# Performance work log

Hardware: AMD Instinct MI355X
Metric: run time of the kernel (lower is better)

The kernel has to match this reference:

```python
import math
import jax, jax.numpy as jnp
import numpy as np

D_MODEL = 1024
N_HEADS = 16
HEAD_DIM = D_MODEL // N_HEADS
D_FF = 4096
N_LAYERS = 4
VOCAB = 2048
NUM_GROUPS = 15
CACHE_LEN = 17  # positions 0..16
EPS = 1e-6


def rmsnorm(x, w):
    return x * w * jax.lax.rsqrt(jnp.mean(x * x, axis=-1, keepdims=True) + EPS)


def rope(x, pos):
    # x: [S, H, hd], pos: [S] int
    hd = x.shape[-1]
    inv = 1.0 / (10000.0 ** (jnp.arange(0, hd, 2, dtype=jnp.float32) / hd))
    ang = pos[:, None].astype(jnp.float32) * inv  # [S, hd/2]
    cos = jnp.cos(ang)[:, None, :]
    sin = jnp.sin(ang)[:, None, :]
    x1, x2 = x[..., ::2], x[..., 1::2]
    return jnp.stack([x1 * cos - x2 * sin, x1 * sin + x2 * cos], axis=-1).reshape(x.shape)


def transformer_step(x, positions, kc, vc, wq, wk, wv, wo, w1, w2, w3, ln1, ln2, lnf):
    # x: [S, d]; positions: [S] contiguous; kc/vc: [L, H, T, hd] KV caches
    S = x.shape[0]
    cache_pos = jnp.arange(CACHE_LEN)
    mask = cache_pos[None, None, :] <= positions[None, :, None]  # causal vs cache [1,S,T]
    start = positions[0]
    for l in range(N_LAYERS):
        h = rmsnorm(x, ln1[l])
        q = rope((h @ wq[l].T).reshape(S, N_HEADS, HEAD_DIM), positions)
        k = rope((h @ wk[l].T).reshape(S, N_HEADS, HEAD_DIM), positions)
        v = (h @ wv[l].T).reshape(S, N_HEADS, HEAD_DIM)
        kc = jax.lax.dynamic_update_slice(kc, k.transpose(1, 0, 2)[None], (l, 0, start, 0))
        vc = jax.lax.dynamic_update_slice(vc, v.transpose(1, 0, 2)[None], (l, 0, start, 0))
        scores = jnp.einsum('shd,htd->hst', q, kc[l]) / math.sqrt(HEAD_DIM)
        p = jax.nn.softmax(jnp.where(mask, scores, -1e30), axis=-1)
        attn = jnp.einsum('hst,htd->shd', p, vc[l]).reshape(S, D_MODEL)
        x = x + attn @ wo[l].T
        h = rmsnorm(x, ln2[l])
        x = x + (jax.nn.silu(h @ w1[l].T) * (h @ w3[l].T)) @ w2[l].T
    return rmsnorm(x, lnf), kc, vc


def forward(talker_hidden, code_0_embed, wq, wk, wv, wo, w1, w2, w3, ln1, ln2, lnf, heads, embeds):
    kc = jnp.zeros((N_LAYERS, N_HEADS, CACHE_LEN, HEAD_DIM), jnp.float32)
    vc = kc
    # prefill: [talker_hidden; code_0_embed] at positions 0,1
    x0 = jnp.concatenate([talker_hidden[0], code_0_embed[0]], axis=0)  # [2, d]
    h, kc, vc = transformer_step(x0, jnp.arange(2), kc, vc, wq, wk, wv, wo, w1, w2, w3, ln1, ln2, lnf)
    hidden = h[-1:]  # last-token hidden [1, d]

    def step(carry, xs):
        hidden, kc, vc = carry
        head, etab, pos = xs  # head/etab: [V, d]
        logits = hidden @ head.T          # [1, V]
        code = jnp.argmax(logits, axis=-1)  # [1]
        emb = etab[code]                   # [1, d]
        nh, kc, vc = transformer_step(emb, pos[None], kc, vc, wq, wk, wv, wo, w1, w2, w3, ln1, ln2, lnf)
        return (nh, kc, vc), (logits[0], emb[0])

    (_, _, _), (all_logits, embs) = jax.lax.scan(
        step, (hidden, kc, vc), (heads, embeds, jnp.arange(2, 2 + NUM_GROUPS)))
    embed_sum = code_0_embed.reshape(-1) + embs.sum(0)
    return all_logits, embed_sum  # [15, V], [d]


def setup_inputs() -> dict:
    key = jax.random.key(0)
    ks = jax.random.split(key, 16)
    s = 0.02
    f32 = jnp.float32
    return {
        'talker_hidden': jax.random.normal(ks[0], (1, 1, D_MODEL), f32),
        'code_0_embed': jax.random.normal(ks[1], (1, 1, D_MODEL), f32),
        'wq': jax.random.normal(ks[2], (N_LAYERS, D_MODEL, D_MODEL), f32) * s,
        'wk': jax.random.normal(ks[3], (N_LAYERS, D_MODEL, D_MODEL), f32) * s,
        'wv': jax.random.normal(ks[4], (N_LAYERS, D_MODEL, D_MODEL), f32) * s,
        'wo': jax.random.normal(ks[5], (N_LAYERS, D_MODEL, D_MODEL), f32) * s,
        'w1': jax.random.normal(ks[6], (N_LAYERS, D_FF, D_MODEL), f32) * s,
        'w2': jax.random.normal(ks[7], (N_LAYERS, D_MODEL, D_FF), f32) * s,
        'w3': jax.random.normal(ks[8], (N_LAYERS, D_FF, D_MODEL), f32) * s,
        'ln1': jnp.ones((N_LAYERS, D_MODEL), f32),
        'ln2': jnp.ones((N_LAYERS, D_MODEL), f32),
        'lnf': jnp.ones((D_MODEL,), f32),
        'heads': jax.random.normal(ks[9], (NUM_GROUPS, VOCAB, D_MODEL), f32) * s,
        'embeds': jax.random.normal(ks[10], (NUM_GROUPS, VOCAB, D_MODEL), f32) * s,
    }


def reference(talker_hidden, code_0_embed, wq, wk, wv, wo, w1, w2, w3, ln1, ln2, lnf, heads, embeds):
    return forward(talker_hidden, code_0_embed, wq, wk, wv, wo, w1, w2, w3, ln1, ln2, lnf, heads, embeds)
```

## Files before the change

### kernel.cpp

```cpp
#include <hip/hip_runtime.h>
#include <hip/hip_bf16.h>
#include <math.h>

#define D_MODEL 1024
#define N_HEADS 16
#define HEAD_DIM 64
#define D_FF 4096
#define N_LAYERS 4
#define VOCAB 2048
#define NUM_GROUPS 15
#define CACHE_LEN 17
#define EPS 1e-6f

typedef unsigned short ushort8v __attribute__((ext_vector_type(8)));

__device__ __forceinline__ float bf2f(unsigned short u) {
  union { unsigned int i; float f; } c;
  c.i = ((unsigned int)u) << 16;
  return c.f;
}

__device__ __forceinline__ unsigned short f2bf(float f) {
  union { float f; unsigned int i; } c;
  c.f = f;
  unsigned int r = (c.i + 0x7fffu + ((c.i >> 16) & 1u)) >> 16;
  return (unsigned short)r;
}

__device__ __forceinline__ float wred(float v) {
#pragma unroll
  for (int o = 32; o > 0; o >>= 1) v += __shfl_xor(v, o, 64);
  return v;
}

template <int NT>
__device__ __forceinline__ void block_rms_scale(const float* __restrict__ x, int S,
                                                float* s_scale, float* s_tmp) {
  for (int s = 0; s < S; ++s) {
    float p = 0.f;
    for (int j = threadIdx.x; j < D_MODEL; j += NT) {
      float v = x[s * D_MODEL + j];
      p += v * v;
    }
    p = wred(p);
    if ((threadIdx.x & 63) == 0) s_tmp[threadIdx.x >> 6] = p;
    __syncthreads();
    if (threadIdx.x == 0) {
      float t = 0.f;
#pragma unroll
      for (int w = 0; w < NT / 64; ++w) t += s_tmp[w];
      s_scale[s] = rsqrtf(t / (float)D_MODEL + EPS);
    }
    __syncthreads();
  }
}

template <int NIT>
__device__ __forceinline__ void load_act_scaled(const float* __restrict__ x,
                                                const float* __restrict__ ln,
                                                float scale, float* a) {
  int lane = threadIdx.x & 63;
  const float4* xv = (const float4*)x;
  const float4* lv = (const float4*)ln;
#pragma unroll
  for (int it = 0; it < NIT; ++it) {
    float4 v0 = xv[it * 128 + lane * 2];
    float4 v1 = xv[it * 128 + lane * 2 + 1];
    float4 l0 = lv[it * 128 + lane * 2];
    float4 l1 = lv[it * 128 + lane * 2 + 1];
    a[it * 8 + 0] = v0.x * l0.x * scale;
    a[it * 8 + 1] = v0.y * l0.y * scale;
    a[it * 8 + 2] = v0.z * l0.z * scale;
    a[it * 8 + 3] = v0.w * l0.w * scale;
    a[it * 8 + 4] = v1.x * l1.x * scale;
    a[it * 8 + 5] = v1.y * l1.y * scale;
    a[it * 8 + 6] = v1.z * l1.z * scale;
    a[it * 8 + 7] = v1.w * l1.w * scale;
  }
}

template <typename WT, int NIT>
__device__ __forceinline__ float dot_cached(const WT* __restrict__ wrow, const float* a) {
  int lane = threadIdx.x & 63;
  float acc = 0.f;
  if constexpr (sizeof(WT) == 2) {
    const ushort8v* w8 = (const ushort8v*)wrow;
#pragma unroll
    for (int it = 0; it < NIT; ++it) {
      ushort8v w = w8[it * 64 + lane];
#pragma unroll
      for (int c = 0; c < 8; ++c) acc = fmaf(bf2f(w[c]), a[it * 8 + c], acc);
    }
  } else {
    const float4* w4 = (const float4*)wrow;
#pragma unroll
    for (int it = 0; it < NIT; ++it) {
      float4 b0 = w4[it * 128 + lane * 2];
      float4 b1 = w4[it * 128 + lane * 2 + 1];
      acc = fmaf(b0.x, a[it * 8 + 0], acc);
      acc = fmaf(b0.y, a[it * 8 + 1], acc);
      acc = fmaf(b0.z, a[it * 8 + 2], acc);
      acc = fmaf(b0.w, a[it * 8 + 3], acc);
      acc = fmaf(b1.x, a[it * 8 + 4], acc);
      acc = fmaf(b1.y, a[it * 8 + 5], acc);
      acc = fmaf(b1.z, a[it * 8 + 6], acc);
      acc = fmaf(b1.w, a[it * 8 + 7], acc);
    }
  }
  return wred(acc);
}

template <typename WT, int NIT>
__device__ __forceinline__ float dot_stream(const WT* __restrict__ wrow,
                                            const float* __restrict__ act) {
  int lane = threadIdx.x & 63;
  const float4* av = (const float4*)act;
  float acc = 0.f;
  if constexpr (sizeof(WT) == 2) {
    const ushort8v* w8 = (const ushort8v*)wrow;
#pragma unroll
    for (int it = 0; it < NIT; ++it) {
      ushort8v w = w8[it * 64 + lane];
      float4 v0 = av[it * 128 + lane * 2];
      float4 v1 = av[it * 128 + lane * 2 + 1];
      acc = fmaf(bf2f(w[0]), v0.x, acc);
      acc = fmaf(bf2f(w[1]), v0.y, acc);
      acc = fmaf(bf2f(w[2]), v0.z, acc);
      acc = fmaf(bf2f(w[3]), v0.w, acc);
      acc = fmaf(bf2f(w[4]), v1.x, acc);
      acc = fmaf(bf2f(w[5]), v1.y, acc);
      acc = fmaf(bf2f(w[6]), v1.z, acc);
      acc = fmaf(bf2f(w[7]), v1.w, acc);
    }
  } else {
    const float4* w4 = (const float4*)wrow;
#pragma unroll
    for (int it = 0; it < NIT; ++it) {
      float4 b0 = w4[it * 128 + lane * 2];
      float4 b1 = w4[it * 128 + lane * 2 + 1];
      float4 v0 = av[it * 128 + lane * 2];
      float4 v1 = av[it * 128 + lane * 2 + 1];
      acc = fmaf(b0.x, v0.x, acc);
      acc = fmaf(b0.y, v0.y, acc);
      acc = fmaf(b0.z, v0.z, acc);
      acc = fmaf(b0.w, v0.w, acc);
      acc = fmaf(b1.x, v1.x, acc);
      acc = fmaf(b1.y, v1.y, acc);
      acc = fmaf(b1.z, v1.z, acc);
      acc = fmaf(b1.w, v1.w, acc);
    }
  }
  return wred(acc);
}


__global__ void k_convert(const float* __restrict__ src, unsigned short* __restrict__ dst,
                          size_t n8) {
  size_t stride = (size_t)gridDim.x * blockDim.x;
  const float4* s4 = (const float4*)src;
  ushort8v* d8 = (ushort8v*)dst;
  for (size_t i = (size_t)blockIdx.x * blockDim.x + threadIdx.x; i < n8; i += stride) {
    float4 a = s4[2 * i];
    float4 b = s4[2 * i + 1];
    ushort8v o;
    o[0] = f2bf(a.x); o[1] = f2bf(a.y); o[2] = f2bf(a.z); o[3] = f2bf(a.w);
    o[4] = f2bf(b.x); o[5] = f2bf(b.y); o[6] = f2bf(b.z); o[7] = f2bf(b.w);
    d8[i] = o;
  }
}

__global__ void k_setup(const float* __restrict__ th, const float* __restrict__ c0,
                        float* __restrict__ x, float* __restrict__ esum) {
  int j = blockIdx.x * 256 + threadIdx.x;
  if (j < D_MODEL) {
    x[j] = th[j];
    x[D_MODEL + j] = c0[j];
    esum[j] = c0[j];
  }
}

template <typename WT>
__global__ __launch_bounds__(256) void k_qkv(
    const float* __restrict__ x, const float* __restrict__ ln,
    const WT* __restrict__ wq, const WT* __restrict__ wk, const WT* __restrict__ wv,
    float* __restrict__ qout, float* __restrict__ kcl, float* __restrict__ vcl,
    int S, int start) {
  __shared__ float s_scale[2];
  __shared__ float s_tmp[4];
  block_rms_scale<256>(x, S, s_scale, s_tmp);
  int lane = threadIdx.x & 63;
  int wid = blockIdx.x * 4 + (threadIdx.x >> 6);
  int m = wid >> 9;
  int p = wid & 511;
  const WT* W = (m == 0) ? wq : (m == 1) ? wk : wv;
  const WT* w0 = W + (size_t)(2 * p) * D_MODEL;
  const WT* w1 = w0 + D_MODEL;
  int h = (2 * p) >> 6;
  int dd = (2 * p) & 63;
  for (int s = 0; s < S; ++s) {
    float a[16];
    load_act_scaled<2>(x + s * D_MODEL, ln, s_scale[s], a);
    float d0 = dot_cached<WT, 2>(w0, a);
    float d1 = dot_cached<WT, 2>(w1, a);
    int pos = start + s;
    if (lane == 0) {
      if (m == 2) {
        vcl[(h * CACHE_LEN + pos) * HEAD_DIM + dd] = d0;
        vcl[(h * CACHE_LEN + pos) * HEAD_DIM + dd + 1] = d1;
      } else {
        int i = dd >> 1;
        float inv = powf(10000.f, -(float)(2 * i) / 64.f);
        float ang = (float)pos * inv;
        float c = cosf(ang), sn = sinf(ang);
        float o0 = d0 * c - d1 * sn;
        float o1 = d0 * sn + d1 * c;
        if (m == 0) {
          qout[s * D_MODEL + 2 * p] = o0;
          qout[s * D_MODEL + 2 * p + 1] = o1;
        } else {
          kcl[(h * CACHE_LEN + pos) * HEAD_DIM + dd] = o0;
          kcl[(h * CACHE_LEN + pos) * HEAD_DIM + dd + 1] = o1;
        }
      }
    }
  }
}

__global__ __launch_bounds__(64) void k_attn(const float* __restrict__ q,
                                             const float* __restrict__ kcl,
                                             const float* __restrict__ vcl,
                                             float* __restrict__ attnb, int S,
                                             int start) {
  int h = blockIdx.x;
  int lane = threadIdx.x;
  __shared__ float sp[CACHE_LEN];
  for (int s = 0; s < S; ++s) {
    int pos = start + s;
    float qd = q[s * D_MODEL + h * HEAD_DIM + lane];
    for (int t = 0; t <= pos; ++t) {
      float prod = qd * kcl[(h * CACHE_LEN + t) * HEAD_DIM + lane];
      float sum = wred(prod);
      if (lane == 0) sp[t] = sum * 0.125f;
    }
    __syncthreads();
    if (lane == 0) {
      float mx = -1e30f;
      for (int t = 0; t <= pos; ++t) mx = fmaxf(mx, sp[t]);
      float sm = 0.f;
      for (int t = 0; t <= pos; ++t) {
        float e = expf(sp[t] - mx);
        sp[t] = e;
        sm += e;
      }
      float r = 1.f / sm;
      for (int t = 0; t <= pos; ++t) sp[t] *= r;
    }
    __syncthreads();
    float acc = 0.f;
    for (int t = 0; t <= pos; ++t)
      acc = fmaf(sp[t], vcl[(h * CACHE_LEN + t) * HEAD_DIM + lane], acc);
    attnb[s * D_MODEL + h * HEAD_DIM + lane] = acc;
    __syncthreads();
  }
}

template <typename WT>
__global__ __launch_bounds__(256) void k_wores(const float* __restrict__ attnb,
                                               const WT* __restrict__ wo,
                                               float* __restrict__ x, int S) {
  int wid = blockIdx.x * 4 + (threadIdx.x >> 6);
  const WT* wrow = wo + (size_t)wid * D_MODEL;
  for (int s = 0; s < S; ++s) {
    float d = dot_stream<WT, 2>(wrow, attnb + s * D_MODEL);
    if ((threadIdx.x & 63) == 0) x[s * D_MODEL + wid] += d;
  }
}

template <typename WT>
__global__ __launch_bounds__(256) void k_ffnup(const float* __restrict__ x,
                                               const float* __restrict__ ln,
                                               const WT* __restrict__ w1,
                                               const WT* __restrict__ w3,
                                               float* __restrict__ ff, int S) {
  __shared__ float s_scale[2];
  __shared__ float s_tmp[4];
  block_rms_scale<256>(x, S, s_scale, s_tmp);
  int lane = threadIdx.x & 63;
  int wid = blockIdx.x * 4 + (threadIdx.x >> 6);
  for (int s = 0; s < S; ++s) {
    float a[16];
    load_act_scaled<2>(x + s * D_MODEL, ln, s_scale[s], a);
#pragma unroll
    for (int jj = 0; jj < 2; ++jj) {
      int j = wid + jj * 2048;
      float g = dot_cached<WT, 2>(w1 + (size_t)j * D_MODEL, a);
      float u = dot_cached<WT, 2>(w3 + (size_t)j * D_MODEL, a);
      if (lane == 0) ff[s * D_FF + j] = (g / (1.f + expf(-g))) * u;
    }
  }
}

template <typename WT>
__global__ __launch_bounds__(256) void k_ffdown(const float* __restrict__ ff,
                                                const WT* __restrict__ w2,
                                                float* __restrict__ x, int S) {
  int wid = blockIdx.x * 4 + (threadIdx.x >> 6);
  const WT* wrow = w2 + (size_t)wid * D_FF;
  for (int s = 0; s < S; ++s) {
    float d = dot_stream<WT, 8>(wrow, ff + s * D_FF);
    if ((threadIdx.x & 63) == 0) x[s * D_MODEL + wid] += d;
  }
}

__global__ __launch_bounds__(256) void k_logits(const float* __restrict__ x, int row,
                                                const float* __restrict__ lnf,
                                                const float* __restrict__ head,
                                                float* __restrict__ out_g,
                                                float* __restrict__ lbuf) {
  __shared__ float s_scale[2];
  __shared__ float s_tmp[4];
  block_rms_scale<256>(x + row * D_MODEL, 1, s_scale, s_tmp);
  int lane = threadIdx.x & 63;
  int wid = blockIdx.x * 4 + (threadIdx.x >> 6);
  float a[16];
  load_act_scaled<2>(x + row * D_MODEL, lnf, s_scale[0], a);
  float d = dot_cached<float, 2>(head + (size_t)wid * D_MODEL, a);
  if (lane == 0) {
    out_g[wid] = d;
    lbuf[wid] = d;
  }
}

__global__ __launch_bounds__(256) void k_argmax_gather(
    const float* __restrict__ lbuf, const float* __restrict__ etab,
    float* __restrict__ x, float* __restrict__ esum, float* __restrict__ out_esum,
    int is_last) {
  __shared__ float bval[256];
  __shared__ int bidx[256];
  float best = -1e38f;
  int bi = 0;
  for (int j = threadIdx.x; j < VOCAB; j += 256) {
    float v = lbuf[j];
    if (v > best) {
      best = v;
      bi = j;
    }
  }
  bval[threadIdx.x] = best;
  bidx[threadIdx.x] = bi;
  __syncthreads();
  for (int off = 128; off > 0; off >>= 1) {
    if (threadIdx.x < off) {
      float v2 = bval[threadIdx.x + off];
      int i2 = bidx[threadIdx.x + off];
      float v1 = bval[threadIdx.x];
      int i1 = bidx[threadIdx.x];
      if (v2 > v1 || (v2 == v1 && i2 < i1)) {
        bval[threadIdx.x] = v2;
        bidx[threadIdx.x] = i2;
      }
    }
    __syncthreads();
  }
  int code = bidx[0];
  const float* emb = etab + (size_t)code * D_MODEL;
  for (int j = threadIdx.x; j < D_MODEL; j += 256) {
    float e = emb[j];
    x[j] = e;
    float ns = esum[j] + e;
    esum[j] = ns;
    if (is_last) out_esum[j] = ns;
  }
}


template <typename WT>
static void run_model(const WT* wq, const WT* wk, const WT* wv, const WT* wo,
                      const WT* w1, const WT* w2, const WT* w3, const float* th,
                      const float* c0, const float* ln1, const float* ln2,
                      const float* lnf, const float* heads, const float* embeds,
                      float* out, float* fs, hipStream_t stream) {
  float* x = fs;
  float* qb = fs + 2048;
  float* attnb = fs + 4096;
  float* ff = fs + 6144;
  float* lbuf = fs + 14336;
  float* esum = fs + 16384;
  float* kc = fs + 17408;
  float* vc = fs + 87040;

  k_setup<<<4, 256, 0, stream>>>(th, c0, x, esum);

  auto run_layers = [&](int S, int start) {
    for (int l = 0; l < N_LAYERS; ++l) {
      const WT* wq_l = wq + (size_t)l * D_MODEL * D_MODEL;
      const WT* wk_l = wk + (size_t)l * D_MODEL * D_MODEL;
      const WT* wv_l = wv + (size_t)l * D_MODEL * D_MODEL;
      const WT* wo_l = wo + (size_t)l * D_MODEL * D_MODEL;
      const WT* w1_l = w1 + (size_t)l * D_FF * D_MODEL;
      const WT* w2_l = w2 + (size_t)l * D_MODEL * D_FF;
      const WT* w3_l = w3 + (size_t)l * D_FF * D_MODEL;
      float* kcl = kc + (size_t)l * N_HEADS * CACHE_LEN * HEAD_DIM;
      float* vcl = vc + (size_t)l * N_HEADS * CACHE_LEN * HEAD_DIM;
      k_qkv<WT><<<384, 256, 0, stream>>>(x, ln1 + l * D_MODEL, wq_l, wk_l, wv_l, qb,
                                         kcl, vcl, S, start);
      k_attn<<<16, 64, 0, stream>>>(qb, kcl, vcl, attnb, S, start);
      k_wores<WT><<<256, 256, 0, stream>>>(attnb, wo_l, x, S);
      k_ffnup<WT><<<512, 256, 0, stream>>>(x, ln2 + l * D_MODEL, w1_l, w3_l, ff, S);
      k_ffdown<WT><<<256, 256, 0, stream>>>(ff, w2_l, x, S);
    }
  };

  run_layers(2, 0);

  for (int g = 0; g < NUM_GROUPS; ++g) {
    int row = (g == 0) ? 1 : 0;
    k_logits<<<512, 256, 0, stream>>>(x, row, lnf, heads + (size_t)g * VOCAB * D_MODEL,
                                      out + (size_t)g * VOCAB, lbuf);
    k_argmax_gather<<<1, 256, 0, stream>>>(lbuf, embeds + (size_t)g * VOCAB * D_MODEL,
                                           x, esum, out + (size_t)NUM_GROUPS * VOCAB,
                                           g == NUM_GROUPS - 1);
    if (g < NUM_GROUPS - 1) run_layers(1, 2 + g);
  }
}

extern "C" void kernel_launch(void* const* d_in, const int* in_sizes, int n_in,
                              void* d_out, int out_size, void* d_ws, size_t ws_size,
                              hipStream_t stream) {
  const float* th = (const float*)d_in[0];
  const float* c0 = (const float*)d_in[1];
  const float* wq = (const float*)d_in[2];
  const float* wk = (const float*)d_in[3];
  const float* wv = (const float*)d_in[4];
  const float* wo = (const float*)d_in[5];
  const float* w1 = (const float*)d_in[6];
  const float* w2 = (const float*)d_in[7];
  const float* w3 = (const float*)d_in[8];
  const float* ln1 = (const float*)d_in[9];
  const float* ln2 = (const float*)d_in[10];
  const float* lnf = (const float*)d_in[11];
  const float* heads = (const float*)d_in[12];
  const float* embeds = (const float*)d_in[13];
  float* out = (float*)d_out;

  const size_t QKVO = (size_t)N_LAYERS * D_MODEL * D_MODEL;
  const size_t FFW = (size_t)N_LAYERS * D_FF * D_MODEL;
  const size_t W_ELEMS = 4 * QKVO + 3 * FFW;
  const size_t SCRATCH_FLOATS = 156672;
  const size_t NEED = W_ELEMS * 2 + SCRATCH_FLOATS * 4;

  if (ws_size >= NEED) {
    unsigned short* wb = (unsigned short*)d_ws;
    unsigned short* bwq = wb;
    unsigned short* bwk = wb + QKVO;
    unsigned short* bwv = wb + 2 * QKVO;
    unsigned short* bwo = wb + 3 * QKVO;
    unsigned short* bw1 = wb + 4 * QKVO;
    unsigned short* bw3 = wb + 4 * QKVO + FFW;
    unsigned short* bw2 = wb + 4 * QKVO + 2 * FFW;
    float* fs = (float*)(wb + W_ELEMS);

    k_convert<<<2048, 256, 0, stream>>>(wq, bwq, QKVO / 8);
    k_convert<<<2048, 256, 0, stream>>>(wk, bwk, QKVO / 8);
    k_convert<<<2048, 256, 0, stream>>>(wv, bwv, QKVO / 8);
    k_convert<<<2048, 256, 0, stream>>>(wo, bwo, QKVO / 8);
    k_convert<<<2048, 256, 0, stream>>>(w1, bw1, FFW / 8);
    k_convert<<<2048, 256, 0, stream>>>(w3, bw3, FFW / 8);
    k_convert<<<2048, 256, 0, stream>>>(w2, bw2, FFW / 8);

    run_model<unsigned short>(bwq, bwk, bwv, bwo, bw1, bw2, bw3, th, c0, ln1, ln2,
                              lnf, heads, embeds, out, fs, stream);
  } else {
    float* fs = (float*)d_ws;
    run_model<float>(wq, wk, wv, wo, w1, w2, w3, th, c0, ln1, ln2, lnf, heads,
                     embeds, out, fs, stream);
  }
}
```

Measured before the change: 1.922 ms.

## Fuse entire decode loop into one persistent cooperative kernel with grid barriers

Replaces the many per-layer kernel launches (qkv, attention, wo, ffn up/down, logits, argmax, weight conversion) with a single cooperative persistent kernel of 256 blocks of 1024 threads that steps through phases separated by a software grid barrier. Attention is fused with the output projection, and argmax plus embedding gather is folded into each block's first layer. The aim is to remove launch overhead and inter-kernel gaps across roughly a hundred small launches. In exchange it depends on atomic spin barriers, and each phase now has a fixed work split that may leave some waves idle.

Measured after the change: 5.654 ms. +194.2%, slower.

```diff
diff --git a/kernel.cpp b/kernel.cpp
--- a/kernel.cpp
+++ b/kernel.cpp
@@ -11,6 +11,8 @@
 #define NUM_GROUPS 15
 #define CACHE_LEN 17
 #define EPS 1e-6f
+#define NB 256
+#define NT 1024
 
 typedef unsigned short ushort8v __attribute__((ext_vector_type(8)));
 
@@ -33,50 +35,68 @@
   return v;
 }
 
-template <int NT>
-__device__ __forceinline__ void block_rms_scale(const float* __restrict__ x, int S,
-                                                float* s_scale, float* s_tmp) {
-  for (int s = 0; s < S; ++s) {
-    float p = 0.f;
-    for (int j = threadIdx.x; j < D_MODEL; j += NT) {
-      float v = x[s * D_MODEL + j];
-      p += v * v;
-    }
-    p = wred(p);
-    if ((threadIdx.x & 63) == 0) s_tmp[threadIdx.x >> 6] = p;
-    __syncthreads();
-    if (threadIdx.x == 0) {
-      float t = 0.f;
-#pragma unroll
-      for (int w = 0; w < NT / 64; ++w) t += s_tmp[w];
-      s_scale[s] = rsqrtf(t / (float)D_MODEL + EPS);
-    }
-    __syncthreads();
-  }
-}
-
-template <int NIT>
-__device__ __forceinline__ void load_act_scaled(const float* __restrict__ x,
-                                                const float* __restrict__ ln,
-                                                float scale, float* a) {
+__device__ __forceinline__ float wredmax(float v) {
+#pragma unroll
+  for (int o = 32; o > 0; o >>= 1) v = fmaxf(v, __shfl_xor(v, o, 64));
+  return v;
+}
+
+struct Sh {
+  float attn[2][D_MODEL];
+  float red[32];
+  float scale[2];
+  float bval[16];
+  int bidx[16];
+  int code;
+};
+
+__device__ __forceinline__ void gsync(unsigned* bar, unsigned& tgt) {
+  tgt += NB;
+  __syncthreads();
+  if (threadIdx.x == 0) {
+    __threadfence();
+    atomicAdd(bar, 1u);
+    while (__hip_atomic_load(bar, __ATOMIC_RELAXED, __HIP_MEMORY_SCOPE_AGENT) < tgt)
+      __builtin_amdgcn_s_sleep(1);
+    __threadfence();
+  }
+  __syncthreads();
+}
+
+__device__ __forceinline__ void block_rms(const float* __restrict__ h, int s, Sh& sh) {
+  int tid = threadIdx.x;
+  float v = h[tid];
+  float p = wred(v * v);
+  if ((tid & 63) == 0) sh.red[tid >> 6] = p;
+  __syncthreads();
+  if (tid == 0) {
+    float t = 0.f;
+#pragma unroll
+    for (int w = 0; w < 16; ++w) t += sh.red[w];
+    sh.scale[s] = rsqrtf(t * (1.f / D_MODEL) + EPS);
+  }
+  __syncthreads();
+}
+
+__device__ __forceinline__ void load_act_off(const float* __restrict__ x,
+                                             const float* __restrict__ ln,
+                                             float scale, int off512, float* a) {
   int lane = threadIdx.x & 63;
-  const float4* xv = (const float4*)x;
-  const float4* lv = (const float4*)ln;
-#pragma unroll
-  for (int it = 0; it < NIT; ++it) {
-    float4 v0 = xv[it * 128 + lane * 2];
-    float4 v1 = xv[it * 128 + lane * 2 + 1];
-    float4 l0 = lv[it * 128 + lane * 2];
-    float4 l1 = lv[it * 128 + lane * 2 + 1];
-    a[it * 8 + 0] = v0.x * l0.x * scale;
-    a[it * 8 + 1] = v0.y * l0.y * scale;
-    a[it * 8 + 2] = v0.z * l0.z * scale;
-    a[it * 8 + 3] = v0.w * l0.w * scale;
-    a[it * 8 + 4] = v1.x * l1.x * scale;
-    a[it * 8 + 5] = v1.y * l1.y * scale;
-    a[it * 8 + 6] = v1.z * l1.z * scale;
-    a[it * 8 + 7] = v1.w * l1.w * scale;
-  }
+  const float4* xv = (const float4*)(x + off512 * 512);
+  const float4* lv = (const float4*)(ln + off512 * 512);
+  float4 v0 = xv[lane * 2], v1 = xv[lane * 2 + 1];
+  float4 l0 = lv[lane * 2], l1 = lv[lane * 2 + 1];
+  a[0] = v0.x * l0.x * scale; a[1] = v0.y * l0.y * scale;
+  a[2] = v0.z * l0.z * scale; a[3] = v0.w * l0.w * scale;
+  a[4] = v1.x * l1.x * scale; a[5] = v1.y * l1.y * scale;
+  a[6] = v1.z * l1.z * scale; a[7] = v1.w * l1.w * scale;
+}
+
+__device__ __forceinline__ void load_act(const float* __restrict__ x,
+                                         const float* __restrict__ ln, float scale,
+                                         float* a) {
+  load_act_off(x, ln, scale, 0, a);
+  load_act_off(x, ln, scale, 1, a + 8);
 }
 
 template <typename WT, int NIT>
@@ -153,13 +173,40 @@
   return wred(acc);
 }
 
-
-__global__ void k_convert(const float* __restrict__ src, unsigned short* __restrict__ dst,
-                          size_t n8) {
-  size_t stride = (size_t)gridDim.x * blockDim.x;
+__device__ __forceinline__ int block_argmax(const float* __restrict__ lbuf, Sh& sh) {
+  int tid = threadIdx.x, lane = tid & 63, wv_ = tid >> 6;
+  float v0 = lbuf[tid];
+  int i0 = tid;
+  float v1 = lbuf[tid + 1024];
+  if (v1 > v0) { v0 = v1; i0 = tid + 1024; }
+#pragma unroll
+  for (int o = 32; o > 0; o >>= 1) {
+    float v2 = __shfl_xor(v0, o, 64);
+    int i2 = __shfl_xor(i0, o, 64);
+    if (v2 > v0 || (v2 == v0 && i2 < i0)) { v0 = v2; i0 = i2; }
+  }
+  if (lane == 0) { sh.bval[wv_] = v0; sh.bidx[wv_] = i0; }
+  __syncthreads();
+  if (tid == 0) {
+    float b = sh.bval[0];
+    int bi = sh.bidx[0];
+#pragma unroll
+    for (int w = 1; w < 16; ++w) {
+      float v = sh.bval[w];
+      int i = sh.bidx[w];
+      if (v > b || (v == b && i < bi)) { b = v; bi = i; }
+    }
+    sh.code = bi;
+  }
+  __syncthreads();
+  return sh.code;
+}
+
+__device__ __forceinline__ void conv_arr(const float* __restrict__ src,
+                                         unsigned short* __restrict__ dst, size_t n8) {
   const float4* s4 = (const float4*)src;
   ushort8v* d8 = (ushort8v*)dst;
-  for (size_t i = (size_t)blockIdx.x * blockDim.x + threadIdx.x; i < n8; i += stride) {
+  for (size_t i = (size_t)blockIdx.x * NT + threadIdx.x; i < n8; i += (size_t)NB * NT) {
     float4 a = s4[2 * i];
     float4 b = s4[2 * i + 1];
     ushort8v o;
@@ -169,310 +216,292 @@
   }
 }
 
-__global__ void k_setup(const float* __restrict__ th, const float* __restrict__ c0,
-                        float* __restrict__ x, float* __restrict__ esum) {
-  int j = blockIdx.x * 256 + threadIdx.x;
-  if (j < D_MODEL) {
-    x[j] = th[j];
-    x[D_MODEL + j] = c0[j];
-    esum[j] = c0[j];
-  }
-}
-
-template <typename WT>
-__global__ __launch_bounds__(256) void k_qkv(
-    const float* __restrict__ x, const float* __restrict__ ln,
-    const WT* __restrict__ wq, const WT* __restrict__ wk, const WT* __restrict__ wv,
-    float* __restrict__ qout, float* __restrict__ kcl, float* __restrict__ vcl,
-    int S, int start) {
-  __shared__ float s_scale[2];
-  __shared__ float s_tmp[4];
-  block_rms_scale<256>(x, S, s_scale, s_tmp);
-  int lane = threadIdx.x & 63;
-  int wid = blockIdx.x * 4 + (threadIdx.x >> 6);
-  int m = wid >> 9;
-  int p = wid & 511;
-  const WT* W = (m == 0) ? wq : (m == 1) ? wk : wv;
-  const WT* w0 = W + (size_t)(2 * p) * D_MODEL;
-  const WT* w1 = w0 + D_MODEL;
-  int h = (2 * p) >> 6;
-  int dd = (2 * p) & 63;
-  for (int s = 0; s < S; ++s) {
-    float a[16];
-    load_act_scaled<2>(x + s * D_MODEL, ln, s_scale[s], a);
-    float d0 = dot_cached<WT, 2>(w0, a);
-    float d1 = dot_cached<WT, 2>(w1, a);
-    int pos = start + s;
-    if (lane == 0) {
-      if (m == 2) {
-        vcl[(h * CACHE_LEN + pos) * HEAD_DIM + dd] = d0;
-        vcl[(h * CACHE_LEN + pos) * HEAD_DIM + dd + 1] = d1;
-      } else {
-        int i = dd >> 1;
-        float inv = powf(10000.f, -(float)(2 * i) / 64.f);
-        float ang = (float)pos * inv;
-        float c = cosf(ang), sn = sinf(ang);
-        float o0 = d0 * c - d1 * sn;
-        float o1 = d0 * sn + d1 * c;
-        if (m == 0) {
-          qout[s * D_MODEL + 2 * p] = o0;
-          qout[s * D_MODEL + 2 * p + 1] = o1;
-        } else {
-          kcl[(h * CACHE_LEN + pos) * HEAD_DIM + dd] = o0;
-          kcl[(h * CACHE_LEN + pos) * HEAD_DIM + dd + 1] = o1;
+struct KParams {
+  const float *th, *c0, *ln1, *ln2, *lnf, *heads, *embeds;
+  const float *fwq, *fwk, *fwv, *fwo, *fw1, *fw2, *fw3;
+  unsigned short *bwq, *bwk, *bwv, *bwo, *bw1, *bw2, *bw3;
+  float *out, *x, *qb, *ff, *lbuf, *esum, *kc, *vc;
+  unsigned* bar;
+};
+
+template <int BF> struct WSel;
+template <> struct WSel<1> { using T = unsigned short; };
+template <> struct WSel<0> { using T = float; };
+
+__global__ void k_zero(unsigned* bar) {
+  if (threadIdx.x == 0) *bar = 0;
+}
+
+template <int BF>
+__global__ __launch_bounds__(NT, 4) void mega(KParams P) {
+  using WT = typename WSel<BF>::T;
+  __shared__ Sh sh;
+  unsigned tgt = 0;
+  const int tid = threadIdx.x, lane = tid & 63, wv_ = tid >> 6;
+
+  const WT* wq = BF ? (const WT*)P.bwq : (const WT*)P.fwq;
+  const WT* wk = BF ? (const WT*)P.bwk : (const WT*)P.fwk;
+  const WT* wv = BF ? (const WT*)P.bwv : (const WT*)P.fwv;
+  const WT* wo = BF ? (const WT*)P.bwo : (const WT*)P.fwo;
+  const WT* w1 = BF ? (const WT*)P.bw1 : (const WT*)P.fw1;
+  const WT* w2 = BF ? (const WT*)P.bw2 : (const WT*)P.fw2;
+  const WT* w3 = BF ? (const WT*)P.bw3 : (const WT*)P.fw3;
+
+  const size_t QKVO = (size_t)N_LAYERS * D_MODEL * D_MODEL;
+  const size_t FFW = (size_t)N_LAYERS * D_FF * D_MODEL;
+
+  if constexpr (BF) {
+    conv_arr(P.fwq, P.bwq, QKVO / 8);
+    conv_arr(P.fwk, P.bwk, QKVO / 8);
+    conv_arr(P.fwv, P.bwv, QKVO / 8);
+    conv_arr(P.fwo, P.bwo, QKVO / 8);
+    conv_arr(P.fw1, P.bw1, FFW / 8);
+    conv_arr(P.fw3, P.bw3, FFW / 8);
+    conv_arr(P.fw2, P.bw2, FFW / 8);
+  }
+  if (blockIdx.x == 0) {
+    P.x[tid] = P.th[tid];
+    P.x[D_MODEL + tid] = P.c0[tid];
+    P.esum[tid] = P.c0[tid];
+  }
+  gsync(P.bar, tgt);
+
+  auto qkv_phase = [&](const float* hin, int S, int start, const float* ln,
+                       const WT* Wq, const WT* Wk, const WT* Wv, float* kcl,
+                       float* vcl) {
+    for (int s = 0; s < S; ++s) block_rms(hin + s * D_MODEL, s, sh);
+    if (wv_ < 6) {
+      int p = blockIdx.x * 6 + wv_;
+      int m = p / 512, pp = p & 511;
+      const WT* W = (m == 0) ? Wq : (m == 1) ? Wk : Wv;
+      const WT* r0 = W + (size_t)(2 * pp) * D_MODEL;
+      const WT* r1 = r0 + D_MODEL;
+      int h = (2 * pp) >> 6, dd = (2 * pp) & 63;
+      for (int s = 0; s < S; ++s) {
+        float a[16];
+        load_act(hin + s * D_MODEL, ln, sh.scale[s], a);
+        float d0 = dot_cached<WT, 2>(r0, a);
+        float d1 = dot_cached<WT, 2>(r1, a);
+        int pos = start + s;
+        if (lane == 0) {
+          if (m == 2) {
+            vcl[(h * CACHE_LEN + pos) * HEAD_DIM + dd] = d0;
+            vcl[(h * CACHE_LEN + pos) * HEAD_DIM + dd + 1] = d1;
+          } else {
+            int i = dd >> 1;
+            float inv = powf(10000.f, -(float)(2 * i) / 64.f);
+            float ang = (float)pos * inv;
+            float c = cosf(ang), sn = sinf(ang);
+            float o0 = d0 * c - d1 * sn;
+            float o1 = d0 * sn + d1 * c;
+            if (m == 0) {
+              P.qb[s * D_MODEL + 2 * pp] = o0;
+              P.qb[s * D_MODEL + 2 * pp + 1] = o1;
+            } else {
+              kcl[(h * CACHE_LEN + pos) * HEAD_DIM + dd] = o0;
+              kcl[(h * CACHE_LEN + pos) * HEAD_DIM + dd + 1] = o1;
+            }
+          }
         }
       }
     }
-  }
-}
-
-__global__ __launch_bounds__(64) void k_attn(const float* __restrict__ q,
-                                             const float* __restrict__ kcl,
-                                             const float* __restrict__ vcl,
-                                             float* __restrict__ attnb, int S,
-                                             int start) {
-  int h = blockIdx.x;
-  int lane = threadIdx.x;
-  __shared__ float sp[CACHE_LEN];
-  for (int s = 0; s < S; ++s) {
-    int pos = start + s;
-    float qd = q[s * D_MODEL + h * HEAD_DIM + lane];
-    for (int t = 0; t <= pos; ++t) {
-      float prod = qd * kcl[(h * CACHE_LEN + t) * HEAD_DIM + lane];
-      float sum = wred(prod);
-      if (lane == 0) sp[t] = sum * 0.125f;
+  };
+
+  auto aw_phase = [&](int S, int start, const WT* Wo, const float* kcl,
+                      const float* vcl) {
+    int h = wv_;
+    for (int s = 0; s < S; ++s) {
+      int pos = start + s;
+      float qd = P.qb[s * D_MODEL + h * HEAD_DIM + lane];
+      float sc = -1e30f;
+      for (int t = 0; t <= pos; ++t) {
+        float sum = wred(qd * kcl[(h * CACHE_LEN + t) * HEAD_DIM + lane]);
+        if (lane == t) sc = sum * 0.125f;
+      }
+      float mx = wredmax(lane <= pos ? sc : -1e30f);
+      float e = (lane <= pos) ? expf(sc - mx) : 0.f;
+      float den = wred(e);
+      float pr = e / den;
+      float acc = 0.f;
+      for (int t = 0; t <= pos; ++t)
+        acc = fmaf(__shfl(pr, t, 64), vcl[(h * CACHE_LEN + t) * HEAD_DIM + lane], acc);
+      sh.attn[s][h * HEAD_DIM + lane] = acc;
     }
     __syncthreads();
-    if (lane == 0) {
-      float mx = -1e30f;
-      for (int t = 0; t <= pos; ++t) mx = fmaxf(mx, sp[t]);
-      float sm = 0.f;
-      for (int t = 0; t <= pos; ++t) {
-        float e = expf(sp[t] - mx);
-        sp[t] = e;
-        sm += e;
+    if (wv_ < 8) {
+      int rr = wv_ >> 1, q = wv_ & 1;
+      int row = blockIdx.x * 4 + rr;
+      const WT* wrow = Wo + (size_t)row * D_MODEL;
+      for (int s = 0; s < S; ++s) {
+        float part = dot_stream<WT, 1>(wrow + q * 512, &sh.attn[s][q * 512]);
+        if (lane == 0) sh.red[s * 16 + wv_] = part;
       }
-      float r = 1.f / sm;
-      for (int t = 0; t <= pos; ++t) sp[t] *= r;
     }
     __syncthreads();
-    float acc = 0.f;
-    for (int t = 0; t <= pos; ++t)
-      acc = fmaf(sp[t], vcl[(h * CACHE_LEN + t) * HEAD_DIM + lane], acc);
-    attnb[s * D_MODEL + h * HEAD_DIM + lane] = acc;
+    if (tid < 4 * S) {
+      int s = tid >> 2, rr = tid & 3;
+      P.x[s * D_MODEL + blockIdx.x * 4 + rr] +=
+          sh.red[s * 16 + rr * 2] + sh.red[s * 16 + rr * 2 + 1];
+    }
+  };
+
+  auto ffup_phase = [&](int S, const float* ln, const WT* W1, const WT* W3) {
+    for (int s = 0; s < S; ++s) block_rms(P.x + s * D_MODEL, s, sh);
+    int j = blockIdx.x * 16 + wv_;
+    const WT* r1 = W1 + (size_t)j * D_MODEL;
+    const WT* r3 = W3 + (size_t)j * D_MODEL;
+    for (int s = 0; s < S; ++s) {
+      float a[16];
+      load_act(P.x + s * D_MODEL, ln, sh.scale[s], a);
+      float g = dot_cached<WT, 2>(r1, a);
+      float u = dot_cached<WT, 2>(r3, a);
+      if (lane == 0) P.ff[s * D_FF + j] = (g / (1.f + expf(-g))) * u;
+    }
+  };
+
+  auto ffdown_phase = [&](int S, const WT* W2) {
+    int rr = wv_ >> 2, q = wv_ & 3;
+    int row = blockIdx.x * 4 + rr;
+    const WT* wrow = W2 + (size_t)row * D_FF;
+    for (int s = 0; s < S; ++s) {
+      float pt = dot_stream<WT, 2>(wrow + q * 1024, P.ff + s * D_FF + q * 1024);
+      if (lane == 0) sh.red[s * 16 + wv_] = pt;
+    }
     __syncthreads();
-  }
-}
-
-template <typename WT>
-__global__ __launch_bounds__(256) void k_wores(const float* __restrict__ attnb,
-                                               const WT* __restrict__ wo,
-                                               float* __restrict__ x, int S) {
-  int wid = blockIdx.x * 4 + (threadIdx.x >> 6);
-  const WT* wrow = wo + (size_t)wid * D_MODEL;
-  for (int s = 0; s < S; ++s) {
-    float d = dot_stream<WT, 2>(wrow, attnb + s * D_MODEL);
-    if ((threadIdx.x & 63) == 0) x[s * D_MODEL + wid] += d;
-  }
-}
-
-template <typename WT>
-__global__ __launch_bounds__(256) void k_ffnup(const float* __restrict__ x,
-                                               const float* __restrict__ ln,
-                                               const WT* __restrict__ w1,
-                                               const WT* __restrict__ w3,
-                                               float* __restrict__ ff, int S) {
-  __shared__ float s_scale[2];
-  __shared__ float s_tmp[4];
-  block_rms_scale<256>(x, S, s_scale, s_tmp);
-  int lane = threadIdx.x & 63;
-  int wid = blockIdx.x * 4 + (threadIdx.x >> 6);
-  for (int s = 0; s < S; ++s) {
-    float a[16];
-    load_act_scaled<2>(x + s * D_MODEL, ln, s_scale[s], a);
-#pragma unroll
-    for (int jj = 0; jj < 2; ++jj) {
-      int j = wid + jj * 2048;
-      float g = dot_cached<WT, 2>(w1 + (size_t)j * D_MODEL, a);
-      float u = dot_cached<WT, 2>(w3 + (size_t)j * D_MODEL, a);
-      if (lane == 0) ff[s * D_FF + j] = (g / (1.f + expf(-g))) * u;
-    }
-  }
-}
-
-template <typename WT>
-__global__ __launch_bounds__(256) void k_ffdown(const float* __restrict__ ff,
-                                                const WT* __restrict__ w2,
-                                                float* __restrict__ x, int S) {
-  int wid = blockIdx.x * 4 + (threadIdx.x >> 6);
-  const WT* wrow = w2 + (size_t)wid * D_FF;
-  for (int s = 0; s < S; ++s) {
-    float d = dot_stream<WT, 8>(wrow, ff + s * D_FF);
-    if ((threadIdx.x & 63) == 0) x[s * D_MODEL + wid] += d;
-  }
-}
-
-__global__ __launch_bounds__(256) void k_logits(const float* __restrict__ x, int row,
-                                                const float* __restrict__ lnf,
-                                                const float* __restrict__ head,
-                                                float* __restrict__ out_g,
-                                                float* __restrict__ lbuf) {
-  __shared__ float s_scale[2];
-  __shared__ float s_tmp[4];
-  block_rms_scale<256>(x + row * D_MODEL, 1, s_scale, s_tmp);
-  int lane = threadIdx.x & 63;
-  int wid = blockIdx.x * 4 + (threadIdx.x >> 6);
-  float a[16];
-  load_act_scaled<2>(x + row * D_MODEL, lnf, s_scale[0], a);
-  float d = dot_cached<float, 2>(head + (size_t)wid * D_MODEL, a);
-  if (lane == 0) {
-    out_g[wid] = d;
-    lbuf[wid] = d;
-  }
-}
-
-__global__ __launch_bounds__(256) void k_argmax_gather(
-    const float* __restrict__ lbuf, const float* __restrict__ etab,
-    float* __restrict__ x, float* __restrict__ esum, float* __restrict__ out_esum,
-    int is_last) {
-  __shared__ float bval[256];
-  __shared__ int bidx[256];
-  float best = -1e38f;
-  int bi = 0;
-  for (int j = threadIdx.x; j < VOCAB; j += 256) {
-    float v = lbuf[j];
-    if (v > best) {
-      best = v;
-      bi = j;
-    }
-  }
-  bval[threadIdx.x] = best;
-  bidx[threadIdx.x] = bi;
-  __syncthreads();
-  for (int off = 128; off > 0; off >>= 1) {
-    if (threadIdx.x < off) {
-      float v2 = bval[threadIdx.x + off];
-      int i2 = bidx[threadIdx.x + off];
-      float v1 = bval[threadIdx.x];
-      int i1 = bidx[threadIdx.x];
-      if (v2 > v1 || (v2 == v1 && i2 < i1)) {
-        bval[threadIdx.x] = v2;
-        bidx[threadIdx.x] = i2;
+    if (tid < 4 * S) {
+      int s = tid >> 2, rr2 = tid & 3;
+      float v = sh.red[s * 16 + rr2 * 4] + sh.red[s * 16 + rr2 * 4 + 1] +
+                sh.red[s * 16 + rr2 * 4 + 2] + sh.red[s * 16 + rr2 * 4 + 3];
+      P.x[s * D_MODEL + blockIdx.x * 4 + rr2] += v;
+    }
+  };
+
+  auto logits_phase = [&](int row, const float* head, float* outg) {
+    block_rms(P.x + row * D_MODEL, 0, sh);
+    int j = blockIdx.x * 8 + (wv_ >> 1);
+    int q = wv_ & 1;
+    float a[8];
+    load_act_off(P.x + row * D_MODEL, P.lnf, sh.scale[0], q, a);
+    float part = dot_cached<float, 1>(head + (size_t)j * D_MODEL + q * 512, a);
+    if (lane == 0) sh.red[wv_] = part;
+    __syncthreads();
+    if (tid < 8) {
+      int j2 = blockIdx.x * 8 + tid;
+      float d = sh.red[tid * 2] + sh.red[tid * 2 + 1];
+      P.lbuf[j2] = d;
+      outg[j2] = d;
+    }
+  };
+
+  auto full_step = [&](int S, int start, bool am, const float* etab) {
+    for (int l = 0; l < N_LAYERS; ++l) {
+      const WT* Wq = wq + (size_t)l * D_MODEL * D_MODEL;
+      const WT* Wk = wk + (size_t)l * D_MODEL * D_MODEL;
+      const WT* Wv = wv + (size_t)l * D_MODEL * D_MODEL;
+      const WT* Wo = wo + (size_t)l * D_MODEL * D_MODEL;
+      const WT* W1 = w1 + (size_t)l * D_FF * D_MODEL;
+      const WT* W2 = w2 + (size_t)l * D_FF * D_MODEL;
+      const WT* W3 = w3 + (size_t)l * D_FF * D_MODEL;
+      float* kcl = P.kc + (size_t)l * N_HEADS * CACHE_LEN * HEAD_DIM;
+      float* vcl = P.vc + (size_t)l * N_HEADS * CACHE_LEN * HEAD_DIM;
+      const float* hin = P.x;
+      if (am && l == 0) {
+        int code = block_argmax(P.lbuf, sh);
+        hin = etab + (size_t)code * D_MODEL;
+        if (blockIdx.x == 0) {
+          float e = hin[tid];
+          P.x[tid] = e;
+          P.esum[tid] += e;
+        }
       }
-    }
-    __syncthreads();
-  }
-  int code = bidx[0];
-  const float* emb = etab + (size_t)code * D_MODEL;
-  for (int j = threadIdx.x; j < D_MODEL; j += 256) {
-    float e = emb[j];
-    x[j] = e;
-    float ns = esum[j] + e;
-    esum[j] = ns;
-    if (is_last) out_esum[j] = ns;
-  }
-}
-
-
-template <typename WT>
-static void run_model(const WT* wq, const WT* wk, const WT* wv, const WT* wo,
-                      const WT* w1, const WT* w2, const WT* w3, const float* th,
-                      const float* c0, const float* ln1, const float* ln2,
-                      const float* lnf, const float* heads, const float* embeds,
-                      float* out, float* fs, hipStream_t stream) {
-  float* x = fs;
-  float* qb = fs + 2048;
-  float* attnb = fs + 4096;
-  float* ff = fs + 6144;
-  float* lbuf = fs + 14336;
-  float* esum = fs + 16384;
-  float* kc = fs + 17408;
-  float* vc = fs + 87040;
-
-  k_setup<<<4, 256, 0, stream>>>(th, c0, x, esum);
-
-  auto run_layers = [&](int S, int start) {
-    for (int l = 0; l < N_LAYERS; ++l) {
-      const WT* wq_l = wq + (size_t)l * D_MODEL * D_MODEL;
-      const WT* wk_l = wk + (size_t)l * D_MODEL * D_MODEL;
-      const WT* wv_l = wv + (size_t)l * D_MODEL * D_MODEL;
-      const WT* wo_l = wo + (size_t)l * D_MODEL * D_MODEL;
-      const WT* w1_l = w1 + (size_t)l * D_FF * D_MODEL;
-      const WT* w2_l = w2 + (size_t)l * D_MODEL * D_FF;
-      const WT* w3_l = w3 + (size_t)l * D_FF * D_MODEL;
-      float* kcl = kc + (size_t)l * N_HEADS * CACHE_LEN * HEAD_DIM;
-      float* vcl = vc + (size_t)l * N_HEADS * CACHE_LEN * HEAD_DIM;
-      k_qkv<WT><<<384, 256, 0, stream>>>(x, ln1 + l * D_MODEL, wq_l, wk_l, wv_l, qb,
-                                         kcl, vcl, S, start);
-      k_attn<<<16, 64, 0, stream>>>(qb, kcl, vcl, attnb, S, start);
-      k_wores<WT><<<256, 256, 0, stream>>>(attnb, wo_l, x, S);
-      k_ffnup<WT><<<512, 256, 0, stream>>>(x, ln2 + l * D_MODEL, w1_l, w3_l, ff, S);
-      k_ffdown<WT><<<256, 256, 0, stream>>>(ff, w2_l, x, S);
+      qkv_phase(hin, S, start, P.ln1 + l * D_MODEL, Wq, Wk, Wv, kcl, vcl);
+      gsync(P.bar, tgt);
+      aw_phase(S, start, Wo, kcl, vcl);
+      gsync(P.bar, tgt);
+      ffup_phase(S, P.ln2 + l * D_MODEL, W1, W3);
+      gsync(P.bar, tgt);
+      ffdown_phase(S, W2);
+      gsync(P.bar, tgt);
     }
   };
 
-  run_layers(2, 0);
+  full_step(2, 0, false, nullptr);
 
   for (int g = 0; g < NUM_GROUPS; ++g) {
-    int row = (g == 0) ? 1 : 0;
-    k_logits<<<512, 256, 0, stream>>>(x, row, lnf, heads + (size_t)g * VOCAB * D_MODEL,
-                                      out + (size_t)g * VOCAB, lbuf);
-    k_argmax_gather<<<1, 256, 0, stream>>>(lbuf, embeds + (size_t)g * VOCAB * D_MODEL,
-                                           x, esum, out + (size_t)NUM_GROUPS * VOCAB,
-                                           g == NUM_GROUPS - 1);
-    if (g < NUM_GROUPS - 1) run_layers(1, 2 + g);
+    logits_phase(g == 0 ? 1 : 0, P.heads + (size_t)g * VOCAB * D_MODEL,
+                 P.out + (size_t)g * VOCAB);
+    gsync(P.bar, tgt);
+    if (g < NUM_GROUPS - 1) {
+      full_step(1, 2 + g, true, P.embeds + (size_t)g * VOCAB * D_MODEL);
+    } else {
+      if (blockIdx.x == 0) {
+        int code = block_argmax(P.lbuf, sh);
+        const float* emb =
+            P.embeds + (size_t)g * VOCAB * D_MODEL + (size_t)code * D_MODEL;
+        P.out[(size_t)NUM_GROUPS * VOCAB + tid] = P.esum[tid] + emb[tid];
+      }
+    }
   }
 }
 
 extern "C" void kernel_launch(void* const* d_in, const int* in_sizes, int n_in,
                               void* d_out, int out_size, void* d_ws, size_t ws_size,
                               hipStream_t stream) {
-  const float* th = (const float*)d_in[0];
-  const float* c0 = (const float*)d_in[1];
-  const float* wq = (const float*)d_in[2];
-  const float* wk = (const float*)d_in[3];
-  const float* wv = (const float*)d_in[4];
-  const float* wo = (const float*)d_in[5];
-  const float* w1 = (const float*)d_in[6];
-  const float* w2 = (const float*)d_in[7];
-  const float* w3 = (const float*)d_in[8];
-  const float* ln1 = (const float*)d_in[9];
-  const float* ln2 = (const float*)d_in[10];
-  const float* lnf = (const float*)d_in[11];
-  const float* heads = (const float*)d_in[12];
-  const float* embeds = (const float*)d_in[13];
-  float* out = (float*)d_out;
+  KParams P;
+  P.th = (const float*)d_in[0];
+  P.c0 = (const float*)d_in[1];
+  P.fwq = (const float*)d_in[2];
+  P.fwk = (const float*)d_in[3];
+  P.fwv = (const float*)d_in[4];
+  P.fwo = (const float*)d_in[5];
+  P.fw1 = (const float*)d_in[6];
+  P.fw2 = (const float*)d_in[7];
+  P.fw3 = (const float*)d_in[8];
+  P.ln1 = (const float*)d_in[9];
+  P.ln2 = (const float*)d_in[10];
+  P.lnf = (const float*)d_in[11];
+  P.heads = (const float*)d_in[12];
+  P.embeds = (const float*)d_in[13];
+  P.out = (float*)d_out;
 
   const size_t QKVO = (size_t)N_LAYERS * D_MODEL * D_MODEL;
   const size_t FFW = (size_t)N_LAYERS * D_FF * D_MODEL;
   const size_t W_ELEMS = 4 * QKVO + 3 * FFW;
-  const size_t SCRATCH_FLOATS = 156672;
-  const size_t NEED = W_ELEMS * 2 + SCRATCH_FLOATS * 4;
-
-  if (ws_size >= NEED) {
+  const size_t SCRATCH = 2048 + 2048 + 8192 + 2048 + 1024 + 69632 + 69632;
+  const size_t NEED = W_ELEMS * 2 + SCRATCH * 4 + 256;
+
+  float* fs;
+  int use_bf16 = (ws_size >= NEED);
+  if (use_bf16) {
     unsigned short* wb = (unsigned short*)d_ws;
-    unsigned short* bwq = wb;
-    unsigned short* bwk = wb + QKVO;
-    unsigned short* bwv = wb + 2 * QKVO;
-    unsigned short* bwo = wb + 3 * QKVO;
-    unsigned short* bw1 = wb + 4 * QKVO;
-    unsigned short* bw3 = wb + 4 * QKVO + FFW;
-    unsigned short* bw2 = wb + 4 * QKVO + 2 * FFW;
-    float* fs = (float*)(wb + W_ELEMS);
-
-    k_convert<<<2048, 256, 0, stream>>>(wq, bwq, QKVO / 8);
-    k_convert<<<2048, 256, 0, stream>>>(wk, bwk, QKVO / 8);
-    k_convert<<<2048, 256, 0, stream>>>(wv, bwv, QKVO / 8);
-    k_convert<<<2048, 256, 0, stream>>>(wo, bwo, QKVO / 8);
-    k_convert<<<2048, 256, 0, stream>>>(w1, bw1, FFW / 8);
-    k_convert<<<2048, 256, 0, stream>>>(w3, bw3, FFW / 8);
-    k_convert<<<2048, 256, 0, stream>>>(w2, bw2, FFW / 8);
-
-    run_model<unsigned short>(bwq, bwk, bwv, bwo, bw1, bw2, bw3, th, c0, ln1, ln2,
-                              lnf, heads, embeds, out, fs, stream);
+    P.bwq = wb;
+    P.bwk = wb + QKVO;
+    P.bwv = wb + 2 * QKVO;
+    P.bwo = wb + 3 * QKVO;
+    P.bw1 = wb + 4 * QKVO;
+    P.bw3 = wb + 4 * QKVO + FFW;
+    P.bw2 = wb + 4 * QKVO + 2 * FFW;
+    fs = (float*)(wb + W_ELEMS);
   } else {
-    float* fs = (float*)d_ws;
-    run_model<float>(wq, wk, wv, wo, w1, w2, w3, th, c0, ln1, ln2, lnf, heads,
-                     embeds, out, fs, stream);
-  }
-}
+    P.bwq = P.bwk = P.bwv = P.bwo = P.bw1 = P.bw2 = P.bw3 = nullptr;
+    fs = (float*)d_ws;
+  }
+  P.x = fs;
+  P.qb = fs + 2048;
+  P.ff = fs + 4096;
+  P.lbuf = fs + 12288;
+  P.esum = fs + 14336;
+  P.kc = fs + 15360;
+  P.vc = fs + 84992;
+  P.bar = (unsigned*)(fs + SCRATCH);
+
+  k_zero<<<1, 64, 0, stream>>>(P.bar);
+  void* args[] = {&P};
+  if (use_bf16) {
+    hipLaunchCooperativeKernel(reinterpret_cast<void*>(&mega<1>), dim3(NB), dim3(NT),
+                               args, 0, stream);
+  } else {
+    hipLaunchCooperativeKernel(reinterpret_cast<void*>(&mega<0>), dim3(NB), dim3(NT),
+                               args, 0, stream);
+  }
+}
```
